# Optimization experiments

Measured on AMD Instinct MI355X. Metric: run time of the kernel, lower is better.

The kernel has to match this reference:

```python
import jax, jax.numpy as jnp
import numpy as np

L = 3        # number of GatedGCN layers
N = 30000    # nodes
E = 480000   # edges (avg degree 16)
D = 128      # hidden dim (= in_dim = out_dim)
IN = 128     # input feature dim
G = 64       # graphs in batch
C = 10       # classes


def setup_inputs() -> dict:
    key = jax.random.key(0)
    ks = jax.random.split(key, 32)
    s = 0.05  # weight scale to keep activations / sigmoid gates in a sane range
    inp = {
        "h": jax.random.normal(ks[0], (N, IN), jnp.float32),
        "e": jax.random.normal(ks[1], (E, IN), jnp.float32),
        "snorm_n": jax.random.uniform(ks[2], (N, 1), jnp.float32),
        "snorm_e": jax.random.uniform(ks[3], (E, 1), jnp.float32),
        "src": jax.random.randint(ks[4], (E,), 0, N, jnp.int32),
        "dst": jax.random.randint(ks[5], (E,), 0, N, jnp.int32),
        "graph_id": jnp.sort(jax.random.randint(ks[6], (N,), 0, G, jnp.int32)),
        # input embeddings
        "Wh_emb": jax.random.normal(ks[7], (IN, D), jnp.float32) * s,
        "bh_emb": jnp.zeros((D,), jnp.float32),
        "We_emb": jax.random.normal(ks[8], (IN, D), jnp.float32) * s,
        "be_emb": jnp.zeros((D,), jnp.float32),
        # per-layer A,B,C,D,E linears (stacked over L)
        "WA": jax.random.normal(ks[9], (L, D, D), jnp.float32) * s,
        "bA": jnp.zeros((L, D), jnp.float32),
        "WB": jax.random.normal(ks[10], (L, D, D), jnp.float32) * s,
        "bB": jnp.zeros((L, D), jnp.float32),
        "WC": jax.random.normal(ks[11], (L, D, D), jnp.float32) * s,
        "bC": jnp.zeros((L, D), jnp.float32),
        "WD": jax.random.normal(ks[12], (L, D, D), jnp.float32) * s,
        "bD": jnp.zeros((L, D), jnp.float32),
        "WE": jax.random.normal(ks[13], (L, D, D), jnp.float32) * s,
        "bE": jnp.zeros((L, D), jnp.float32),
        # batch-norm affine params (node / edge)
        "gn_h": jnp.ones((L, D), jnp.float32),
        "bt_h": jnp.zeros((L, D), jnp.float32),
        "gn_e": jnp.ones((L, D), jnp.float32),
        "bt_e": jnp.zeros((L, D), jnp.float32),
        # readout linear
        "Wr": jax.random.normal(ks[14], (D, C), jnp.float32) * s,
        "br": jnp.zeros((C,), jnp.float32),
    }
    return inp


def _bn(x, gamma, beta):
    # training-mode BatchNorm1d: biased batch stats over the node/edge axis
    mu = jnp.mean(x, axis=0)
    var = jnp.var(x, axis=0)
    return (x - mu) * jax.lax.rsqrt(var + 1e-5) * gamma + beta


def reference(h, e, snorm_n, snorm_e, src, dst, graph_id,
              Wh_emb, bh_emb, We_emb, be_emb,
              WA, bA, WB, bB, WC, bC, WD, bD, WE, bE,
              gn_h, bt_h, gn_e, bt_e, Wr, br):
    n_nodes = h.shape[0]
    h = h @ Wh_emb + bh_emb
    e = e @ We_emb + be_emb
    for l in range(WA.shape[0]):
        h_in, e_in = h, e
        Ah = h @ WA[l] + bA[l]
        Bh = h @ WB[l] + bB[l]
        Dh = h @ WD[l] + bD[l]
        Eh = h @ WE[l] + bE[l]
        Ce = e @ WC[l] + bC[l]
        # message: e_ij = Ce + Dh_src + Eh_dst ; gate = sigmoid(e_ij)
        e_new = Ce + Dh[src] + Eh[dst]                       # [E, D]
        sig = jax.nn.sigmoid(e_new)
        # reduce at dst: gated weighted mean of Bh_src
        num = jax.ops.segment_sum(sig * Bh[src], dst, num_segments=n_nodes)
        den = jax.ops.segment_sum(sig, dst, num_segments=n_nodes)
        h_new = Ah + num / (den + 1e-6)
        # graph norm
        h_new = h_new * snorm_n
        e_new = e_new * snorm_e
        # batch norm + ReLU + residual (dropout p=0 -> identity)
        h_new = jax.nn.relu(_bn(h_new, gn_h[l], bt_h[l]))
        e_new = jax.nn.relu(_bn(e_new, gn_e[l], bt_e[l]))
        h = h_in + h_new
        e = e_in + e_new
    # mean_nodes readout per graph, then linear classifier
    sums = jax.ops.segment_sum(h, graph_id, num_segments=G)
    cnt = jax.ops.segment_sum(jnp.ones((n_nodes, 1), h.dtype), graph_id, num_segments=G)
    hg = sums / jnp.maximum(cnt, 1.0)
    return hg @ Wr + br
```

## Files before the change

kernel.cpp:

```cpp
#include <hip/hip_runtime.h>
#include <cstdint>
#include <cstddef>

#define N_NODES  30000
#define N_EDGES  480000
#define N_LAYERS 3
#define N_GRAPHS 64
#define N_CLASS  10
#define NREP     32

typedef __attribute__((ext_vector_type(8))) short short8v;
typedef __attribute__((ext_vector_type(4))) float f32x4;

__device__ __forceinline__ unsigned short f2bf(float x) {
  union { float f; unsigned u; } v; v.f = x;
  unsigned r = v.u + 0x7FFFu + ((v.u >> 16) & 1u);
  return (unsigned short)(r >> 16);
}
__device__ __forceinline__ float bf2f(unsigned short h) {
  union { unsigned u; float f; } v; v.u = ((unsigned)h) << 16;
  return v.f;
}
__device__ __forceinline__ int swzW(int row, int off16) {
  return (row << 8) | (off16 ^ ((row & 7) << 4));
}

__global__ void wconv(const float* __restrict__ Wh, const float* __restrict__ We,
                      const float* __restrict__ WA, const float* __restrict__ WB,
                      const float* __restrict__ WC, const float* __restrict__ WD,
                      const float* __restrict__ WE, unsigned short* __restrict__ Wt)
{
  const int mi  = blockIdx.x >> 6;
  const int idx = (blockIdx.x & 63) * 256 + threadIdx.x;
  const float* src;
  if      (mi == 0) src = Wh;
  else if (mi == 1) src = We;
  else if (mi < 5)  src = WA + (size_t)(mi - 2) * 16384;
  else if (mi < 8)  src = WB + (size_t)(mi - 5) * 16384;
  else if (mi < 11) src = WC + (size_t)(mi - 8) * 16384;
  else if (mi < 14) src = WD + (size_t)(mi - 11) * 16384;
  else              src = WE + (size_t)(mi - 14) * 16384;
  const int k = idx >> 7, n = idx & 127;
  Wt[(size_t)mi * 16384 + (size_t)n * 128 + k] = f2bf(src[idx]);
}

struct GemmArgs {
  const unsigned short* Wt[4];
  const float* bias[4];
  unsigned short* out[4];
};

template<int NMAT, int AMODE>
__global__ __launch_bounds__(256)
void gemm_mm(const void* __restrict__ Ap, GemmArgs g, int M,
             const unsigned short* __restrict__ tb, const float2* __restrict__ pqh,
             unsigned short* __restrict__ hout,
             const unsigned short* __restrict__ WtX, const float* __restrict__ biasX)
{
  __shared__ __align__(16) unsigned char WL[32768];
  unsigned short* Wl = (unsigned short*)WL;
  const int t = threadIdx.x;
  const int w = t >> 6, l = t & 63;
  const int lr = l & 15, lkb = (l >> 4) * 8;
  const int r0 = blockIdx.x * 64;
  const bool vrow = (r0 + w * 16 + lr) < M;
  int arow = r0 + w * 16 + lr; if (arow >= M) arow = M - 1;

  short8v a[4];
  if (AMODE == 2) {
#pragma unroll
    for (int p = 0; p < 8; ++p) {
      const int ci = t + p * 256;
      *(short8v*)(WL + swzW(ci >> 4, (ci & 15) * 16)) = *(const short8v*)(WtX + (size_t)ci * 8);
    }
    const float* A = (const float*)Ap;
#pragma unroll
    for (int kk = 0; kk < 4; ++kk) {
      const float* p = A + (size_t)arow * 128 + kk * 32 + lkb;
      const float4 u = *(const float4*)p;
      const float4 v = *(const float4*)(p + 4);
      short8v av;
      av[0]=f2bf(u.x); av[1]=f2bf(u.y); av[2]=f2bf(u.z); av[3]=f2bf(u.w);
      av[4]=f2bf(v.x); av[5]=f2bf(v.y); av[6]=f2bf(v.z); av[7]=f2bf(v.w);
      a[kk] = av;
    }
    __syncthreads();
    f32x4 acc[8];
#pragma unroll
    for (int ct = 0; ct < 8; ++ct) acc[ct] = (f32x4){0.f, 0.f, 0.f, 0.f};
#pragma unroll
    for (int kk = 0; kk < 4; ++kk)
#pragma unroll
      for (int ct = 0; ct < 8; ++ct) {
        const short8v b = *(const short8v*)(WL + swzW(ct * 16 + lr, kk * 64 + (l >> 4) * 16));
        acc[ct] = __builtin_amdgcn_mfma_f32_16x16x32_bf16(a[kk], b, acc[ct], 0, 0, 0);
      }
    __syncthreads();
#pragma unroll
    for (int ct = 0; ct < 8; ++ct) {
      const float bb = biasX[ct * 16 + lr];
#pragma unroll
      for (int q = 0; q < 4; ++q)
        Wl[(w * 16 + (l >> 4) * 4 + q) * 136 + ct * 16 + lr] = f2bf(acc[ct][q] + bb);
    }
    __syncthreads();
#pragma unroll
    for (int kk = 0; kk < 4; ++kk) {
      a[kk] = *(const short8v*)(Wl + (w * 16 + lr) * 136 + kk * 32 + lkb);
      if (vrow) *(short8v*)(hout + (size_t)arow * 128 + kk * 32 + lkb) = a[kk];
    }
  } else if (AMODE == 1) {
    const unsigned short* A = (const unsigned short*)Ap;
#pragma unroll
    for (int kk = 0; kk < 4; ++kk) {
      const short8v tv = *(const short8v*)(tb + (size_t)arow * 128 + kk * 32 + lkb);
      const short8v hr = *(const short8v*)(A + (size_t)arow * 128 + kk * 32 + lkb);
      short8v av;
#pragma unroll
      for (int j = 0; j < 8; ++j) {
        const float2 PQ = pqh[kk * 32 + lkb + j];
        const float x = bf2f((unsigned short)tv[j]) * PQ.x + PQ.y;
        av[j] = (short)f2bf(bf2f((unsigned short)hr[j]) + fmaxf(x, 0.f));
      }
      a[kk] = av;
      if (vrow) *(short8v*)(hout + (size_t)arow * 128 + kk * 32 + lkb) = av;
    }
  } else {
    const unsigned short* A = (const unsigned short*)Ap;
#pragma unroll
    for (int kk = 0; kk < 4; ++kk)
      a[kk] = *(const short8v*)(A + (size_t)arow * 128 + kk * 32 + lkb);
  }

#pragma unroll
  for (int m = 0; m < NMAT; ++m) {
    if (m || AMODE == 2) __syncthreads();
#pragma unroll
    for (int p = 0; p < 8; ++p) {
      const int ci = t + p * 256;
      *(short8v*)(WL + swzW(ci >> 4, (ci & 15) * 16)) = *(const short8v*)(g.Wt[m] + (size_t)ci * 8);
    }
    __syncthreads();
    f32x4 acc[8];
#pragma unroll
    for (int ct = 0; ct < 8; ++ct) acc[ct] = (f32x4){0.f, 0.f, 0.f, 0.f};
#pragma unroll
    for (int kk = 0; kk < 4; ++kk)
#pragma unroll
      for (int ct = 0; ct < 8; ++ct) {
        const short8v b = *(const short8v*)(WL + swzW(ct * 16 + lr, kk * 64 + (l >> 4) * 16));
        acc[ct] = __builtin_amdgcn_mfma_f32_16x16x32_bf16(a[kk], b, acc[ct], 0, 0, 0);
      }
    __syncthreads();
#pragma unroll
    for (int ct = 0; ct < 8; ++ct) {
      const float bb = g.bias[m][ct * 16 + lr];
#pragma unroll
      for (int q = 0; q < 4; ++q)
        Wl[(w * 16 + (l >> 4) * 4 + q) * 136 + ct * 16 + lr] = f2bf(acc[ct][q] + bb);
    }
    __syncthreads();
    unsigned short* out = g.out[m];
#pragma unroll
    for (int p = 0; p < 4; ++p) {
      const int ci = t + p * 256;
      const int rr = ci >> 4, co = (ci & 15) * 8;
      const int grow = r0 + rr;
      if (grow < M)
        *(short8v*)(out + (size_t)grow * 128 + co) = *(const short8v*)(Wl + rr * 136 + co);
    }
  }
}

template<int LMODE>
__global__ __launch_bounds__(256)
void edge_kern(const float* __restrict__ e_in, const int* __restrict__ csr,
               unsigned short* __restrict__ eres, unsigned short* __restrict__ enew,
               const unsigned short* __restrict__ WtEmb, const float* __restrict__ bEmb,
               const unsigned short* __restrict__ WtC, const float* __restrict__ bC,
               const unsigned short* __restrict__ Dh, const unsigned short* __restrict__ Eh,
               const int* __restrict__ csrc, const int* __restrict__ cdst,
               const float* __restrict__ csne, const float2* __restrict__ pq)
{
  extern __shared__ __align__(16) char smem[];
  char* SM = smem;
  unsigned short* TB = (unsigned short*)((LMODE == 0) ? (smem + 32768) : smem);
  float2* pql = (float2*)(smem + ((LMODE == 0) ? 49664 : 32768));
  const int t = threadIdx.x;
  const int w = t >> 6, l = t & 63;
  const int lr = l & 15, lkb = (l >> 4) * 8;
  const int r0 = blockIdx.x * 64;
  const int pos = r0 + w * 16 + lr;

  short8v a[4];
  f32x4 acc[8];

  if (LMODE == 0) {
#pragma unroll
    for (int p = 0; p < 8; ++p) {
      const int ci = t + p * 256;
      *(short8v*)(SM + swzW(ci >> 4, (ci & 15) * 16)) = *(const short8v*)(WtEmb + (size_t)ci * 8);
    }
#pragma unroll
    for (int p = 0; p < 4; ++p) {
      const int ci = t + p * 256;
      const int rr = ci >> 4, co = (ci & 15) * 8;
      const float* sp = e_in + (size_t)csr[r0 + rr] * 128 + co;
      const float4 u = *(const float4*)sp;
      const float4 v = *(const float4*)(sp + 4);
      short8v av;
      av[0]=f2bf(u.x); av[1]=f2bf(u.y); av[2]=f2bf(u.z); av[3]=f2bf(u.w);
      av[4]=f2bf(v.x); av[5]=f2bf(v.y); av[6]=f2bf(v.z); av[7]=f2bf(v.w);
      *(short8v*)(TB + rr * 132 + co) = av;
    }
    __syncthreads();
#pragma unroll
    for (int kk = 0; kk < 4; ++kk)
      a[kk] = *(const short8v*)(TB + (w * 16 + lr) * 132 + kk * 32 + lkb);
#pragma unroll
    for (int ct = 0; ct < 8; ++ct) acc[ct] = (f32x4){0.f, 0.f, 0.f, 0.f};
#pragma unroll
    for (int kk = 0; kk < 4; ++kk)
#pragma unroll
      for (int ct = 0; ct < 8; ++ct) {
        const short8v b = *(const short8v*)(SM + swzW(ct * 16 + lr, kk * 64 + (l >> 4) * 16));
        acc[ct] = __builtin_amdgcn_mfma_f32_16x16x32_bf16(a[kk], b, acc[ct], 0, 0, 0);
      }
    __syncthreads();
#pragma unroll
    for (int ct = 0; ct < 8; ++ct) {
      const float bb = bEmb[ct * 16 + lr];
#pragma unroll
      for (int q = 0; q < 4; ++q)
        TB[(w * 16 + (l >> 4) * 4 + q) * 132 + ct * 16 + lr] = f2bf(acc[ct][q] + bb);
    }
#pragma unroll
    for (int p = 0; p < 8; ++p) {
      const int ci = t + p * 256;
      *(short8v*)(SM + swzW(ci >> 4, (ci & 15) * 16)) = *(const short8v*)(WtC + (size_t)ci * 8);
    }
    __syncthreads();
#pragma unroll
    for (int kk = 0; kk < 4; ++kk) {
      a[kk] = *(const short8v*)(TB + (w * 16 + lr) * 132 + kk * 32 + lkb);
      *(short8v*)(eres + (size_t)pos * 128 + kk * 32 + lkb) = a[kk];
    }
  } else {
    if (t < 128) pql[t] = pq[t];
#pragma unroll
    for (int p = 0; p < 8; ++p) {
      const int ci = t + p * 256;
      *(short8v*)(SM + swzW(ci >> 4, (ci & 15) * 16)) = *(const short8v*)(WtC + (size_t)ci * 8);
    }
    const float sn = csne[pos];
    short8v ep[4], er[4];
#pragma unroll
    for (int kk = 0; kk < 4; ++kk) {
      ep[kk] = *(const short8v*)(enew + (size_t)pos * 128 + kk * 32 + lkb);
      er[kk] = *(const short8v*)(eres + (size_t)pos * 128 + kk * 32 + lkb);
    }
    __syncthreads();
#pragma unroll
    for (int kk = 0; kk < 4; ++kk) {
      short8v av;
#pragma unroll
      for (int j = 0; j < 8; ++j) {
        const float2 PQ = pql[kk * 32 + lkb + j];
        const float x = bf2f((unsigned short)ep[kk][j]) * sn * PQ.x + PQ.y;
        av[j] = (short)f2bf(bf2f((unsigned short)er[kk][j]) + fmaxf(x, 0.f));
      }
      a[kk] = av;
      if (LMODE == 2)
        *(short8v*)(eres + (size_t)pos * 128 + kk * 32 + lkb) = av;
    }
  }

#pragma unroll
  for (int ct = 0; ct < 8; ++ct) acc[ct] = (f32x4){0.f, 0.f, 0.f, 0.f};
#pragma unroll
  for (int kk = 0; kk < 4; ++kk)
#pragma unroll
    for (int ct = 0; ct < 8; ++ct) {
      const short8v b = *(const short8v*)(SM + swzW(ct * 16 + lr, kk * 64 + (l >> 4) * 16));
      acc[ct] = __builtin_amdgcn_mfma_f32_16x16x32_bf16(a[kk], b, acc[ct], 0, 0, 0);
    }
  __syncthreads();
#pragma unroll
  for (int ct = 0; ct < 8; ++ct) {
    const float bb = bC[ct * 16 + lr];
#pragma unroll
    for (int q = 0; q < 4; ++q)
      TB[(w * 16 + (l >> 4) * 4 + q) * 132 + ct * 16 + lr] = f2bf(acc[ct][q] + bb);
  }
  __syncthreads();
#pragma unroll
  for (int p = 0; p < 4; ++p) {
    const int ci = t + p * 256;
    const int rr = ci >> 4, co = (ci & 15) * 8;
    const int pp = r0 + rr;
    const int s = csrc[pp], d = cdst[pp];
    const short8v ce = *(const short8v*)(TB + rr * 132 + co);
    const short8v dv = *(const short8v*)(Dh + (size_t)s * 128 + co);
    const short8v ev = *(const short8v*)(Eh + (size_t)d * 128 + co);
    short8v ov;
#pragma unroll
    for (int j = 0; j < 8; ++j)
      ov[j] = (short)f2bf(bf2f((unsigned short)ce[j]) + bf2f((unsigned short)dv[j]) + bf2f((unsigned short)ev[j]));
    *(short8v*)(enew + (size_t)pp * 128 + co) = ov;
  }
}

__global__ void hist_kernel(const int* __restrict__ dst, int* __restrict__ cnt, int E)
{
  const int i = blockIdx.x * 256 + threadIdx.x;
  if (i < E) atomicAdd(&cnt[dst[i]], 1);
}

__global__ void scan_kernel(const int* __restrict__ cnt, int* __restrict__ start,
                            int* __restrict__ cursor, int n, int total)
{
  __shared__ int lds[1024];
  const int tid = threadIdx.x;
  const int chunk = (n + 1023) / 1024;
  const int lo = tid * chunk, hi = min(lo + chunk, n);
  int s = 0;
  for (int i = lo; i < hi; ++i) s += cnt[i];
  lds[tid] = s;
  __syncthreads();
  for (int off = 1; off < 1024; off <<= 1) {
    const int v = (tid >= off) ? lds[tid - off] : 0;
    __syncthreads();
    lds[tid] += v;
    __syncthreads();
  }
  int run = (tid == 0) ? 0 : lds[tid - 1];
  for (int i = lo; i < hi; ++i) { start[i] = run; cursor[i] = run; run += cnt[i]; }
  if (tid == 0) start[n] = total;
}

__global__ void scatter_kernel(const int* __restrict__ dst, const int* __restrict__ src,
                               const float* __restrict__ sne, int* __restrict__ cursor,
                               int* __restrict__ csr, int* __restrict__ csrc,
                               int* __restrict__ cdst, float* __restrict__ csne, int E)
{
  const int i = blockIdx.x * 256 + threadIdx.x;
  if (i < E) {
    const int p = atomicAdd(&cursor[dst[i]], 1);
    csr[p] = i; csrc[p] = src[i]; cdst[p] = dst[i]; csne[p] = sne[i];
  }
}

template<int DOE>
__global__ __launch_bounds__(256)
void aggregate(const unsigned short* __restrict__ enew, const unsigned short* __restrict__ Bh,
               const unsigned short* __restrict__ Ah, const float* __restrict__ snorm_n,
               const int* __restrict__ start, const int* __restrict__ csrc,
               const float* __restrict__ csne,
               unsigned short* __restrict__ tbuf, float* __restrict__ statrep)
{
  __shared__ float2 red[16][132];
  const int t = threadIdx.x;
  const int g = t >> 4, q = t & 15;
  const int v = blockIdx.x * 16 + g;
  const int s0 = start[v], s1 = start[v + 1];
  float num[8] = {0,0,0,0,0,0,0,0}, den[8] = {0,0,0,0,0,0,0,0};
  float psE[8] = {0,0,0,0,0,0,0,0}, pqE[8] = {0,0,0,0,0,0,0,0};

  float sn = 0.f;
  short8v ev = {}, bv = {};
  if (s0 < s1) {
    if (DOE) sn = csne[s0];
    ev = *(const short8v*)(enew + (size_t)s0 * 128 + q * 8);
    bv = *(const short8v*)(Bh + (size_t)csrc[s0] * 128 + q * 8);
  }
  for (int i = s0; i < s1; ++i) {
    float snn = 0.f;
    short8v evn = {}, bvn = {};
    if (i + 1 < s1) {
      if (DOE) snn = csne[i + 1];
      evn = *(const short8v*)(enew + (size_t)(i + 1) * 128 + q * 8);
      bvn = *(const short8v*)(Bh + (size_t)csrc[i + 1] * 128 + q * 8);
    }
#pragma unroll
    for (int j = 0; j < 8; ++j) {
      const float en = bf2f((unsigned short)ev[j]);
      const float sg = 1.f / (1.f + __expf(-en));
      num[j] = fmaf(sg, bf2f((unsigned short)bv[j]), num[j]);
      den[j] += sg;
      if (DOE) { const float tv = en * sn; psE[j] += tv; pqE[j] = fmaf(tv, tv, pqE[j]); }
    }
    ev = evn; bv = bvn; sn = snn;
  }
  const float snv = snorm_n[v];
  const short8v av = *(const short8v*)(Ah + (size_t)v * 128 + q * 8);
  float hv[8];
  short8v tout;
#pragma unroll
  for (int j = 0; j < 8; ++j) {
    hv[j] = (bf2f((unsigned short)av[j]) + num[j] / (den[j] + 1e-6f)) * snv;
    tout[j] = (short)f2bf(hv[j]);
  }
  *(short8v*)(tbuf + (size_t)v * 128 + q * 8) = tout;

  float* rep = statrep + (size_t)(blockIdx.x & (NREP - 1)) * 512;
#pragma unroll
  for (int j = 0; j < 8; ++j) red[g][q * 8 + j] = make_float2(hv[j], hv[j] * hv[j]);
  __syncthreads();
  if (t < 128) {
    float s = 0.f, qq = 0.f;
    for (int gg = 0; gg < 16; ++gg) { s += red[gg][t].x; qq += red[gg][t].y; }
    atomicAdd(rep + t, s); atomicAdd(rep + 128 + t, qq);
  }
  if (DOE) {
    __syncthreads();
#pragma unroll
    for (int j = 0; j < 8; ++j) red[g][q * 8 + j] = make_float2(psE[j], pqE[j]);
    __syncthreads();
    if (t < 128) {
      float s = 0.f, qq = 0.f;
      for (int gg = 0; gg < 16; ++gg) { s += red[gg][t].x; qq += red[gg][t].y; }
      atomicAdd(rep + 256 + t, s); atomicAdd(rep + 384 + t, qq);
    }
  }
}

__global__ void finalize_kernel(float* __restrict__ rep, float2* __restrict__ pqh,
                                float2* __restrict__ pqe,
                                const float* __restrict__ gn_h_l, const float* __restrict__ bt_h_l,
                                const float* __restrict__ gn_e_l, const float* __restrict__ bt_e_l,
                                float invN, float invE, int doE)
{
  const int c = threadIdx.x;
  float sH = 0.f, qH = 0.f, sE = 0.f, qE = 0.f;
  for (int r = 0; r < NREP; ++r) {
    float* p = rep + (size_t)r * 512;
    sH += p[c]; qH += p[128 + c]; sE += p[256 + c]; qE += p[384 + c];
    p[c] = 0.f; p[128 + c] = 0.f; p[256 + c] = 0.f; p[384 + c] = 0.f;
  }
  const float muH = sH * invN;
  const float vH  = fmaxf(qH * invN - muH * muH, 0.f);
  const float PH  = rsqrtf(vH + 1e-5f) * gn_h_l[c];
  pqh[c] = make_float2(PH, bt_h_l[c] - muH * PH);
  if (doE) {
    const float muE = sE * invE;
    const float vE  = fmaxf(qE * invE - muE * muE, 0.f);
    const float PE  = rsqrtf(vE + 1e-5f) * gn_e_l[c];
    pqe[c] = make_float2(PE, bt_e_l[c] - muE * PE);
  }
}

__global__ void readout_scatter(const unsigned short* __restrict__ h, const unsigned short* __restrict__ tb,
                                const float2* __restrict__ pqh, const int* __restrict__ gid,
                                float* __restrict__ gsum, int* __restrict__ gcnt, int N)
{
  const int c = threadIdx.x;
  const float2 PQ = pqh[c];
  const int row0 = blockIdx.x * 256;
  int cur = -1, cnt = 0;
  float s = 0.f;
  for (int r = 0; r < 256; ++r) {
    const int v = row0 + r;
    if (v >= N) break;
    const int g = gid[v];
    if (g != cur) {
      if (cur >= 0) {
        atomicAdd(&gsum[(size_t)cur * 128 + c], s);
        if (c == 0) atomicAdd(&gcnt[cur], cnt);
      }
      cur = g; s = 0.f; cnt = 0;
    }
    s += bf2f(h[(size_t)v * 128 + c]) + fmaxf(bf2f(tb[(size_t)v * 128 + c]) * PQ.x + PQ.y, 0.f);
    ++cnt;
  }
  if (cur >= 0) {
    atomicAdd(&gsum[(size_t)cur * 128 + c], s);
    if (c == 0) atomicAdd(&gcnt[cur], cnt);
  }
}

__global__ void readout_final(const float* __restrict__ gsum, const int* __restrict__ gcnt,
                              const float* __restrict__ Wr, const float* __restrict__ br,
                              float* __restrict__ out)
{
  const int g = blockIdx.x;
  const int t = threadIdx.x;
  __shared__ float hg[128];
  const float cnt = fmaxf((float)gcnt[g], 1.f);
  hg[t] = gsum[(size_t)g * 128 + t] / cnt;
  __syncthreads();
  if (t < N_CLASS) {
    float acc = br[t];
    for (int k = 0; k < 128; ++k) acc = fmaf(hg[k], Wr[k * N_CLASS + t], acc);
    out[g * N_CLASS + t] = acc;
  }
}

extern "C" void kernel_launch(void* const* d_in, const int* in_sizes, int n_in,
                              void* d_out, int out_size, void* d_ws, size_t ws_size,
                              hipStream_t stream)
{
  const float* h_in    = (const float*)d_in[0];
  const float* e_in    = (const float*)d_in[1];
  const float* snorm_n = (const float*)d_in[2];
  const float* snorm_e = (const float*)d_in[3];
  const int*   src     = (const int*)d_in[4];
  const int*   dst     = (const int*)d_in[5];
  const int*   gid     = (const int*)d_in[6];
  const float* Wh_emb  = (const float*)d_in[7];
  const float* bh_emb  = (const float*)d_in[8];
  const float* We_emb  = (const float*)d_in[9];
  const float* be_emb  = (const float*)d_in[10];
  const float* WA = (const float*)d_in[11]; const float* bA = (const float*)d_in[12];
  const float* WB = (const float*)d_in[13]; const float* bB = (const float*)d_in[14];
  const float* WC = (const float*)d_in[15]; const float* bC = (const float*)d_in[16];
  const float* WD = (const float*)d_in[17]; const float* bD = (const float*)d_in[18];
  const float* WE = (const float*)d_in[19]; const float* bE = (const float*)d_in[20];
  const float* gn_h = (const float*)d_in[21]; const float* bt_h = (const float*)d_in[22];
  const float* gn_e = (const float*)d_in[23]; const float* bt_e = (const float*)d_in[24];
  const float* Wr = (const float*)d_in[25]; const float* br = (const float*)d_in[26];
  float* out = (float*)d_out;
  (void)in_sizes; (void)n_in; (void)out_size; (void)ws_size;

  char* ws = (char*)d_ws;
  size_t off = 0;
  auto alloc = [&](size_t bytes) -> char* {
    off = (off + 255) & ~(size_t)255;
    char* p = ws + off;
    off += bytes;
    return p;
  };
  const size_t ND = (size_t)N_NODES * 128, ED = (size_t)N_EDGES * 128;
  unsigned short* hbuf = (unsigned short*)alloc(ND * 2);
  unsigned short* ebuf = (unsigned short*)alloc(ED * 2);
  unsigned short* enew = (unsigned short*)alloc(ED * 2);
  unsigned short* Ah   = (unsigned short*)alloc(ND * 2);
  unsigned short* Bh   = (unsigned short*)alloc(ND * 2);
  unsigned short* Dh   = (unsigned short*)alloc(ND * 2);
  unsigned short* Eh   = (unsigned short*)alloc(ND * 2);
  unsigned short* tbuf = (unsigned short*)alloc(ND * 2);
  unsigned short* Wt   = (unsigned short*)alloc((size_t)17 * 16384 * 2);
  float2* pqh          = (float2*)alloc(128 * 8);
  float2* pqe          = (float2*)alloc(128 * 8);
  int* start  = (int*)alloc((size_t)(N_NODES + 1) * 4);
  int* cursor = (int*)alloc((size_t)N_NODES * 4);
  int* csr    = (int*)alloc((size_t)N_EDGES * 4);
  int* csrc   = (int*)alloc((size_t)N_EDGES * 4);
  int* cdst   = (int*)alloc((size_t)N_EDGES * 4);
  float* csne = (float*)alloc((size_t)N_EDGES * 4);
  char* zbase = (char*)alloc(0);
  int*   cnt     = (int*)alloc((size_t)N_NODES * 4);
  float* statrep = (float*)alloc((size_t)NREP * 512 * 4);
  float* gsum    = (float*)alloc((size_t)N_GRAPHS * 128 * 4);
  int*   gcnt    = (int*)alloc((size_t)N_GRAPHS * 4);
  char* zend = (char*)alloc(0);

  hipMemsetAsync(zbase, 0, (size_t)(zend - zbase), stream);

  wconv<<<17 * 64, 256, 0, stream>>>(Wh_emb, We_emb, WA, WB, WC, WD, WE, Wt);

  hist_kernel<<<(N_EDGES + 255) / 256, 256, 0, stream>>>(dst, cnt, N_EDGES);
  scan_kernel<<<1, 1024, 0, stream>>>(cnt, start, cursor, N_NODES, N_EDGES);
  scatter_kernel<<<(N_EDGES + 255) / 256, 256, 0, stream>>>(dst, src, snorm_e, cursor,
                                                            csr, csrc, cdst, csne, N_EDGES);

  const int gbN = (N_NODES + 63) / 64;
  const int gbE = N_EDGES / 64;
  const unsigned SH0 = 49664 + 1024;
  const unsigned SH2 = 32768 + 1024;

  for (int l = 0; l < N_LAYERS; ++l) {
    const size_t bOff = (size_t)l * 128;
    const int doE = (l < N_LAYERS - 1) ? 1 : 0;
    {
      GemmArgs g{};
      g.Wt[0] = Wt + (size_t)(2 + l)  * 16384; g.bias[0] = bA + bOff; g.out[0] = Ah;
      g.Wt[1] = Wt + (size_t)(5 + l)  * 16384; g.bias[1] = bB + bOff; g.out[1] = Bh;
      g.Wt[2] = Wt + (size_t)(11 + l) * 16384; g.bias[2] = bD + bOff; g.out[2] = Dh;
      g.Wt[3] = Wt + (size_t)(14 + l) * 16384; g.bias[3] = bE + bOff; g.out[3] = Eh;
      if (l == 0)
        gemm_mm<4, 2><<<gbN, 256, 0, stream>>>(h_in, g, N_NODES, nullptr, nullptr, hbuf,
                                               Wt + 0 * 16384, bh_emb);
      else
        gemm_mm<4, 1><<<gbN, 256, 0, stream>>>(hbuf, g, N_NODES, tbuf, pqh, hbuf,
                                               nullptr, nullptr);
    }
    const unsigned short* WtC = Wt + (size_t)(8 + l) * 16384;
    if (l == 0)
      edge_kern<0><<<gbE, 256, SH0, stream>>>(e_in, csr, ebuf, enew, Wt + 1 * 16384, be_emb,
                                              WtC, bC + bOff, Dh, Eh, csrc, cdst, csne, nullptr);
    else if (l == 1)
      edge_kern<2><<<gbE, 256, SH2, stream>>>(nullptr, nullptr, ebuf, enew, nullptr, nullptr,
                                              WtC, bC + bOff, Dh, Eh, csrc, cdst, csne, pqe);
    else
      edge_kern<3><<<gbE, 256, SH2, stream>>>(nullptr, nullptr, ebuf, enew, nullptr, nullptr,
                                              WtC, bC + bOff, Dh, Eh, csrc, cdst, csne, pqe);
    if (doE)
      aggregate<1><<<N_NODES / 16, 256, 0, stream>>>(enew, Bh, Ah, snorm_n, start, csrc, csne,
                                                     tbuf, statrep);
    else
      aggregate<0><<<N_NODES / 16, 256, 0, stream>>>(enew, Bh, Ah, snorm_n, start, csrc, csne,
                                                     tbuf, statrep);
    finalize_kernel<<<1, 128, 0, stream>>>(statrep, pqh, pqe, gn_h + bOff, bt_h + bOff,
                                           gn_e + bOff, bt_e + bOff,
                                           1.f / N_NODES, 1.f / N_EDGES, doE);
  }

  readout_scatter<<<(N_NODES + 255) / 256, 128, 0, stream>>>(hbuf, tbuf, pqh, gid, gsum, gcnt, N_NODES);
  readout_final<<<N_GRAPHS, 128, 0, stream>>>(gsum, gcnt, Wr, br, out);
}
```

Measured before the change: 897.8 us.

## Split node GEMM into one block per weight matrix via grid y-dimension

The node GEMM kernel, which looped over four weight matrices per block, now launches a 2D grid so each block computes one matrix output. This gives four times as many blocks on the 30000-row node GEMM for better CU occupancy. The cost is that the A-operand prologue (including the fused embedding GEMM at layer 0 and the BN/ReLU/residual at later layers) is recomputed four times. The h buffer is now double-buffered to avoid read/write races between blocks. Separately, the edge kernel drops its shared-memory staging of the BN scale/shift table and reads it directly from global memory.

```diff
diff --git a/kernel.cpp b/kernel.cpp
--- a/kernel.cpp
+++ b/kernel.cpp
@@ -50,21 +50,23 @@
   unsigned short* out[4];
 };
 
-template<int NMAT, int AMODE>
+template<int AMODE>
 __global__ __launch_bounds__(256)
-void gemm_mm(const void* __restrict__ Ap, GemmArgs g, int M,
-             const unsigned short* __restrict__ tb, const float2* __restrict__ pqh,
-             unsigned short* __restrict__ hout,
-             const unsigned short* __restrict__ WtX, const float* __restrict__ biasX)
+void gemm_one(const void* __restrict__ Ap, GemmArgs g, int M,
+              const unsigned short* __restrict__ tb, const float2* __restrict__ pqh,
+              unsigned short* __restrict__ hout,
+              const unsigned short* __restrict__ WtX, const float* __restrict__ biasX)
 {
   __shared__ __align__(16) unsigned char WL[32768];
   unsigned short* Wl = (unsigned short*)WL;
   const int t = threadIdx.x;
+  const int m = blockIdx.y;
   const int w = t >> 6, l = t & 63;
   const int lr = l & 15, lkb = (l >> 4) * 8;
   const int r0 = blockIdx.x * 64;
   const bool vrow = (r0 + w * 16 + lr) < M;
   int arow = r0 + w * 16 + lr; if (arow >= M) arow = M - 1;
+  const bool wr0 = (m == 0);
 
   short8v a[4];
   if (AMODE == 2) {
@@ -107,8 +109,9 @@
 #pragma unroll
     for (int kk = 0; kk < 4; ++kk) {
       a[kk] = *(const short8v*)(Wl + (w * 16 + lr) * 136 + kk * 32 + lkb);
-      if (vrow) *(short8v*)(hout + (size_t)arow * 128 + kk * 32 + lkb) = a[kk];
-    }
+      if (wr0 && vrow) *(short8v*)(hout + (size_t)arow * 128 + kk * 32 + lkb) = a[kk];
+    }
+    __syncthreads();
   } else if (AMODE == 1) {
     const unsigned short* A = (const unsigned short*)Ap;
 #pragma unroll
@@ -123,7 +126,7 @@
         av[j] = (short)f2bf(bf2f((unsigned short)hr[j]) + fmaxf(x, 0.f));
       }
       a[kk] = av;
-      if (vrow) *(short8v*)(hout + (size_t)arow * 128 + kk * 32 + lkb) = av;
+      if (wr0 && vrow) *(short8v*)(hout + (size_t)arow * 128 + kk * 32 + lkb) = av;
     }
   } else {
     const unsigned short* A = (const unsigned short*)Ap;
@@ -133,42 +136,38 @@
   }
 
 #pragma unroll
-  for (int m = 0; m < NMAT; ++m) {
-    if (m || AMODE == 2) __syncthreads();
-#pragma unroll
-    for (int p = 0; p < 8; ++p) {
-      const int ci = t + p * 256;
-      *(short8v*)(WL + swzW(ci >> 4, (ci & 15) * 16)) = *(const short8v*)(g.Wt[m] + (size_t)ci * 8);
-    }
-    __syncthreads();
-    f32x4 acc[8];
-#pragma unroll
-    for (int ct = 0; ct < 8; ++ct) acc[ct] = (f32x4){0.f, 0.f, 0.f, 0.f};
-#pragma unroll
-    for (int kk = 0; kk < 4; ++kk)
-#pragma unroll
-      for (int ct = 0; ct < 8; ++ct) {
-        const short8v b = *(const short8v*)(WL + swzW(ct * 16 + lr, kk * 64 + (l >> 4) * 16));
-        acc[ct] = __builtin_amdgcn_mfma_f32_16x16x32_bf16(a[kk], b, acc[ct], 0, 0, 0);
-      }
-    __syncthreads();
+  for (int p = 0; p < 8; ++p) {
+    const int ci = t + p * 256;
+    *(short8v*)(WL + swzW(ci >> 4, (ci & 15) * 16)) = *(const short8v*)(g.Wt[m] + (size_t)ci * 8);
+  }
+  __syncthreads();
+  f32x4 acc[8];
+#pragma unroll
+  for (int ct = 0; ct < 8; ++ct) acc[ct] = (f32x4){0.f, 0.f, 0.f, 0.f};
+#pragma unroll
+  for (int kk = 0; kk < 4; ++kk)
 #pragma unroll
     for (int ct = 0; ct < 8; ++ct) {
-      const float bb = g.bias[m][ct * 16 + lr];
-#pragma unroll
-      for (int q = 0; q < 4; ++q)
-        Wl[(w * 16 + (l >> 4) * 4 + q) * 136 + ct * 16 + lr] = f2bf(acc[ct][q] + bb);
-    }
-    __syncthreads();
-    unsigned short* out = g.out[m];
-#pragma unroll
-    for (int p = 0; p < 4; ++p) {
-      const int ci = t + p * 256;
-      const int rr = ci >> 4, co = (ci & 15) * 8;
-      const int grow = r0 + rr;
-      if (grow < M)
-        *(short8v*)(out + (size_t)grow * 128 + co) = *(const short8v*)(Wl + rr * 136 + co);
-    }
+      const short8v b = *(const short8v*)(WL + swzW(ct * 16 + lr, kk * 64 + (l >> 4) * 16));
+      acc[ct] = __builtin_amdgcn_mfma_f32_16x16x32_bf16(a[kk], b, acc[ct], 0, 0, 0);
+    }
+  __syncthreads();
+#pragma unroll
+  for (int ct = 0; ct < 8; ++ct) {
+    const float bb = g.bias[m][ct * 16 + lr];
+#pragma unroll
+    for (int q = 0; q < 4; ++q)
+      Wl[(w * 16 + (l >> 4) * 4 + q) * 136 + ct * 16 + lr] = f2bf(acc[ct][q] + bb);
+  }
+  __syncthreads();
+  unsigned short* out = g.out[m];
+#pragma unroll
+  for (int p = 0; p < 4; ++p) {
+    const int ci = t + p * 256;
+    const int rr = ci >> 4, co = (ci & 15) * 8;
+    const int grow = r0 + rr;
+    if (grow < M)
+      *(short8v*)(out + (size_t)grow * 128 + co) = *(const short8v*)(Wl + rr * 136 + co);
   }
 }
 
@@ -185,7 +184,6 @@
   extern __shared__ __align__(16) char smem[];
   char* SM = smem;
   unsigned short* TB = (unsigned short*)((LMODE == 0) ? (smem + 32768) : smem);
-  float2* pql = (float2*)(smem + ((LMODE == 0) ? 49664 : 32768));
   const int t = threadIdx.x;
   const int w = t >> 6, l = t & 63;
   const int lr = l & 15, lkb = (l >> 4) * 8;
@@ -246,7 +244,6 @@
       *(short8v*)(eres + (size_t)pos * 128 + kk * 32 + lkb) = a[kk];
     }
   } else {
-    if (t < 128) pql[t] = pq[t];
 #pragma unroll
     for (int p = 0; p < 8; ++p) {
       const int ci = t + p * 256;
@@ -259,13 +256,12 @@
       ep[kk] = *(const short8v*)(enew + (size_t)pos * 128 + kk * 32 + lkb);
       er[kk] = *(const short8v*)(eres + (size_t)pos * 128 + kk * 32 + lkb);
     }
-    __syncthreads();
 #pragma unroll
     for (int kk = 0; kk < 4; ++kk) {
       short8v av;
 #pragma unroll
       for (int j = 0; j < 8; ++j) {
-        const float2 PQ = pql[kk * 32 + lkb + j];
+        const float2 PQ = pq[kk * 32 + lkb + j];
         const float x = bf2f((unsigned short)ep[kk][j]) * sn * PQ.x + PQ.y;
         av[j] = (short)f2bf(bf2f((unsigned short)er[kk][j]) + fmaxf(x, 0.f));
       }
@@ -273,6 +269,7 @@
       if (LMODE == 2)
         *(short8v*)(eres + (size_t)pos * 128 + kk * 32 + lkb) = av;
     }
+    __syncthreads();
   }
 
 #pragma unroll
@@ -530,9 +527,10 @@
     return p;
   };
   const size_t ND = (size_t)N_NODES * 128, ED = (size_t)N_EDGES * 128;
-  unsigned short* hbuf = (unsigned short*)alloc(ND * 2);
-  unsigned short* ebuf = (unsigned short*)alloc(ED * 2);
-  unsigned short* enew = (unsigned short*)alloc(ED * 2);
+  unsigned short* hbufA = (unsigned short*)alloc(ND * 2);
+  unsigned short* hbufB = (unsigned short*)alloc(ND * 2);
+  unsigned short* ebuf  = (unsigned short*)alloc(ED * 2);
+  unsigned short* enew  = (unsigned short*)alloc(ED * 2);
   unsigned short* Ah   = (unsigned short*)alloc(ND * 2);
   unsigned short* Bh   = (unsigned short*)alloc(ND * 2);
   unsigned short* Dh   = (unsigned short*)alloc(ND * 2);
@@ -565,8 +563,12 @@
 
   const int gbN = (N_NODES + 63) / 64;
   const int gbE = N_EDGES / 64;
-  const unsigned SH0 = 49664 + 1024;
-  const unsigned SH2 = 32768 + 1024;
+  const dim3 gN(gbN, 4);
+  const unsigned SH0 = 49664;
+  const unsigned SH2 = 32768;
+
+  unsigned short* hcur = hbufA;
+  unsigned short* hnxt = hbufB;
 
   for (int l = 0; l < N_LAYERS; ++l) {
     const size_t bOff = (size_t)l * 128;
@@ -577,12 +579,14 @@
       g.Wt[1] = Wt + (size_t)(5 + l)  * 16384; g.bias[1] = bB + bOff; g.out[1] = Bh;
       g.Wt[2] = Wt + (size_t)(11 + l) * 16384; g.bias[2] = bD + bOff; g.out[2] = Dh;
       g.Wt[3] = Wt + (size_t)(14 + l) * 16384; g.bias[3] = bE + bOff; g.out[3] = Eh;
-      if (l == 0)
-        gemm_mm<4, 2><<<gbN, 256, 0, stream>>>(h_in, g, N_NODES, nullptr, nullptr, hbuf,
-                                               Wt + 0 * 16384, bh_emb);
-      else
-        gemm_mm<4, 1><<<gbN, 256, 0, stream>>>(hbuf, g, N_NODES, tbuf, pqh, hbuf,
-                                               nullptr, nullptr);
+      if (l == 0) {
+        gemm_one<2><<<gN, 256, 0, stream>>>(h_in, g, N_NODES, nullptr, nullptr, hcur,
+                                            Wt + 0 * 16384, bh_emb);
+      } else {
+        gemm_one<1><<<gN, 256, 0, stream>>>(hcur, g, N_NODES, tbuf, pqh, hnxt,
+                                            nullptr, nullptr);
+        unsigned short* tmp = hcur; hcur = hnxt; hnxt = tmp;
+      }
     }
     const unsigned short* WtC = Wt + (size_t)(8 + l) * 16384;
     if (l == 0)
@@ -605,6 +609,6 @@
                                            1.f / N_NODES, 1.f / N_EDGES, doE);
   }
 
-  readout_scatter<<<(N_NODES + 255) / 256, 128, 0, stream>>>(hbuf, tbuf, pqh, gid, gsum, gcnt, N_NODES);
+  readout_scatter<<<(N_NODES + 255) / 256, 128, 0, stream>>>(hcur, tbuf, pqh, gid, gsum, gcnt, N_NODES);
   readout_final<<<N_GRAPHS, 128, 0, stream>>>(gsum, gcnt, Wr, br, out);
 }
```

Measured after the change: 941.1 us. 4.8% more time.
